# Performance work log

Measured on AMD Instinct MI355X. Metric: run time of the kernel, lower is better.

Reference implementation:

```python
import jax, jax.numpy as jnp
import numpy as np

H = 16        # attention heads
KVH = 4       # kv heads (GQA)
D = 128       # qk head_dim = qk_nope(64) + qk_rope(64)
ROPE = 64     # rotary sub-dim
VCH = 128     # v_channels
HID = 2048    # hidden size
E = 8         # routed experts
K = 2         # top-k
EPS = 1e-6
THETA = 10000.0


def rmsnorm(x, w):
    return x * jax.lax.rsqrt(jnp.mean(x * x, axis=-1, keepdims=True) + EPS) * w


def apply_rope(x, pos):
    # x: [T, h, ROPE]; rotate-half convention on the rope sub-dim
    half = ROPE // 2
    inv_freq = 1.0 / (THETA ** (jnp.arange(half, dtype=jnp.float32) / half))
    ang = pos.astype(jnp.float32)[:, None] * inv_freq          # [T, half]
    cos = jnp.cos(ang)[:, None, :]
    sin = jnp.sin(ang)[:, None, :]
    x1, x2 = x[..., :half], x[..., half:]
    return jnp.concatenate([x1 * cos - x2 * sin, x1 * sin + x2 * cos], axis=-1)


def swiglu(x, w_gate, w_up, w_down):
    return (jax.nn.silu(x @ w_gate) * (x @ w_up)) @ w_down


def setup_inputs() -> dict:
    key = jax.random.key(0)
    ks = jax.random.split(key, 16)
    T = 2048
    sc = 0.02
    n = lambda k, s: jax.random.normal(k, s, dtype=jnp.float32) * sc
    return {
        "x": jax.random.normal(ks[0], (T, HID), dtype=jnp.float32),
        "positions": jnp.arange(T, dtype=jnp.int32),
        "ln1_w": jnp.ones((HID,), jnp.float32),
        "qkv_w": n(ks[1], (HID, H * D + KVH * D + KVH * VCH)),
        "qkv_b": n(ks[2], (H * D + KVH * D + KVH * VCH,)),
        "k_ln_w": jnp.ones((D,), jnp.float32),
        "o_w": n(ks[3], (H * VCH, HID)),
        "ln2_w": jnp.ones((HID,), jnp.float32),
        "router_w": n(ks[4], (HID, E)),
        "w1": n(ks[5], (E, HID, 512)),
        "w2": n(ks[6], (E, 512, HID)),
        "w3": n(ks[7], (E, HID, 512)),
        "sw1": n(ks[8], (HID, 1024)),
        "sw2": n(ks[9], (1024, HID)),
        "sw3": n(ks[10], (HID, 1024)),
    }


def reference(x, positions, ln1_w, qkv_w, qkv_b, k_ln_w, o_w, ln2_w,
              router_w, w1, w2, w3, sw1, sw2, sw3):
    T = x.shape[0]
    # --- attention block ---
    h = rmsnorm(x, ln1_w)
    qkv = h @ qkv_w + qkv_b
    q = qkv[:, : H * D].reshape(T, H, D)
    k = qkv[:, H * D : H * D + KVH * D].reshape(T, KVH, D)
    v = qkv[:, H * D + KVH * D :].reshape(T, KVH, VCH)
    k = rmsnorm(k, k_ln_w)  # per-head k_layernorm over head_dim
    # rope applied to the trailing qk_rope_dim of q/k
    q = jnp.concatenate([q[..., : D - ROPE], apply_rope(q[..., D - ROPE :], positions)], -1)
    k = jnp.concatenate([k[..., : D - ROPE], apply_rope(k[..., D - ROPE :], positions)], -1)
    rep = H // KVH
    kf = jnp.repeat(k, rep, axis=1)   # [T, H, D]
    vf = jnp.repeat(v, rep, axis=1)   # [T, H, VCH]
    scale = D ** -0.5
    scores = jnp.einsum("qhd,khd->hqk", q, kf) * scale
    causal = jnp.tril(jnp.ones((T, T), dtype=bool))
    scores = jnp.where(causal[None], scores, jnp.float32(-1e30))
    p = jax.nn.softmax(scores, axis=-1)
    attn = jnp.einsum("hqk,khv->qhv", p, vf).reshape(T, H * VCH)
    x = x + attn @ o_w
    # --- MoE block: shared expert + top-k routed experts ---
    h2 = rmsnorm(x, ln2_w)
    probs = jax.nn.softmax(h2 @ router_w, axis=-1)            # [T, E]
    topw, topi = jax.lax.top_k(probs, K)
    topw = topw / jnp.sum(topw, axis=-1, keepdims=True)        # renormalize top-k
    combine = jnp.sum(jax.nn.one_hot(topi, E, dtype=h2.dtype) * topw[..., None], axis=1)  # [T, E]
    moe = swiglu(h2, sw1, sw3, sw2)                            # shared expert
    for e in range(E):  # small fixed expert count
        moe = moe + combine[:, e : e + 1] * swiglu(h2, w1[e], w3[e], w2[e])
    return x + moe
```

## Files before the change

kernel.cpp:

```cpp
#include <hip/hip_runtime.h>


typedef _Float16 half_t;
typedef _Float16 half8 __attribute__((ext_vector_type(8)));
typedef float    f32x4 __attribute__((ext_vector_type(4)));
typedef float    floatx4 __attribute__((ext_vector_type(4)));

#define T_TOK 2048
#define HIDN  2048
#define NH    16
#define NKVH  4
#define HD    128
#define QKV_N 3072
#define NEXP  8
#define NPAIR_MAX 4608

#define MFMA16(a,b,c) __builtin_amdgcn_mfma_f32_16x16x32_f16(a,b,c,0,0,0)

__device__ __forceinline__ void gload_lds16(const half_t* g, half_t* l) {
    __builtin_amdgcn_global_load_lds(
        (const __attribute__((address_space(1))) void*)g,
        (__attribute__((address_space(3))) void*)l, 16, 0, 0);
}

// ... 14 lines not shown
    for (int o = 32; o; o >>= 1) ss += __shfl_down(ss, o);
    __shared__ float red[4];
    if ((tid & 63) == 0) red[tid >> 6] = ss;
    __syncthreads();
    ss = red[0] + red[1] + red[2] + red[3];
    float rs = rsqrtf(ss * (1.0f / HIDN) + 1e-6f);
    floatx4 w0 = *(const floatx4*)(w + tid * 8);
    floatx4 w1 = *(const floatx4*)(w + tid * 8 + 4);
    float vv[8] = { v0[0]*w0[0], v0[1]*w0[1], v0[2]*w0[2], v0[3]*w0[3],
                    v1[0]*w1[0], v1[1]*w1[1], v1[2]*w1[2], v1[3]*w1[3] };
    half8 hv, lv;
#pragma unroll
    for (int j = 0; j < 8; ++j) {
        float o = vv[j] * rs;
        half_t h = (half_t)o;
        hv[j] = h;
        lv[j] = (half_t)((o - (float)h) * 1024.0f);
    }
    *(half8*)(hi + (size_t)row * HIDN + tid * 8) = hv;
    if (lo) *(half8*)(lo + (size_t)row * HIDN + tid * 8) = lv;
}

__global__ __launch_bounds__(256)
void transpose_split2(const float* __restrict__ src, half_t* __restrict__ dh,
                      half_t* __restrict__ dl, int sstride, int dstride)
{
    __shared__ float tile[32][36];
    const int n0 = blockIdx.x * 32, k0 = blockIdx.y * 32;
    const int tid = threadIdx.x;
    {
        int r = tid >> 3, c = (tid & 7) * 4;
        *(floatx4*)&tile[r][c] =
            *(const floatx4*)(src + (size_t)(k0 + r) * sstride + n0 + c);
    }
    __syncthreads();
    int n = tid & 31, g = tid >> 5, gg = g & 3;
    half8 hv;
    if (g < 4) {
#pragma unroll
        for (int j = 0; j < 8; ++j) hv[j] = (half_t)tile[gg * 8 + j][n];
        *(half8*)(dh + (size_t)(n0 + n) * dstride + k0 + gg * 8) = hv;
    } else {
#pragma unroll
        for (int j = 0; j < 8; ++j) {
            float v = tile[gg * 8 + j][n];
            half_t h = (half_t)v;
            hv[j] = (half_t)((v - (float)h) * 1024.0f);
        }
        *(half8*)(dl + (size_t)(n0 + n) * dstride + k0 + gg * 8) = hv;
    }
}

__global__ __launch_bounds__(256)
void transpose_f16(const float* __restrict__ src, half_t* __restrict__ dh,
                   int sstride, int dstride)
{
// ... 55 lines not shown
    const int tid = threadIdx.x;
    {
        int r = tid >> 3, c = (tid & 7) * 4;
        int k = k0 + r;
        const float* s;
        if (k < 1024) s = sw2 + (size_t)k * HIDN + n0;
        else {
            int e = (k - 1024) >> 9, kk = (k - 1024) & 511;
            s = w2 + ((size_t)e * 512 + kk) * HIDN + n0;
        }
        *(floatx4*)&tile[r][c]      = *(const floatx4*)(s + c);
        *(floatx4*)&tile[r][c + 32] = *(const floatx4*)(s + c + 32);
    }
    __syncthreads();
    int n = tid & 63, g = tid >> 6;
    half8 hv;
#pragma unroll
    for (int j = 0; j < 8; ++j) hv[j] = (half_t)tile[g * 8 + j][n];
    *(half8*)(dst + (size_t)(n0 + n) * 5120 + k0 + g * 8) = hv;
}

__global__ __launch_bounds__(256)
void owu_kernel(const float* __restrict__ ow, const float* __restrict__ ln2w,
                const float* __restrict__ rw, float* __restrict__ owu)
{
    const int k = blockIdx.x * 4 + (threadIdx.x >> 6);
    const int lane = threadIdx.x & 63;
    float acc[NEXP] = {};
    const float* row = ow + (size_t)k * HIDN;
#pragma unroll
    for (int j = 0; j < 8; ++j) {
        int c = j * 256 + lane * 4;
        floatx4 ov = *(const floatx4*)(row + c);
        floatx4 lw = *(const floatx4*)(ln2w + c);
#pragma unroll
        for (int i = 0; i < 4; ++i) {
            float s = ov[i] * lw[i];
            const float* rwc = rw + (size_t)(c + i) * NEXP;
#pragma unroll
            for (int e = 0; e < NEXP; ++e) acc[e] += s * rwc[e];
        }
    }
#pragma unroll
    for (int e = 0; e < NEXP; ++e)
        for (int o = 32; o; o >>= 1) acc[e] += __shfl_down(acc[e], o);
    if (lane == 0) {
#pragma unroll
        for (int e = 0; e < NEXP; ++e) owu[(size_t)k * NEXP + e] = acc[e];
    }
}

template<bool SPLIT, int BM>
__global__ __launch_bounds__(256, 2)
void gemm_f16(const half_t* __restrict__ Ah, const half_t* __restrict__ Al,
              const half_t* __restrict__ Bth, const half_t* __restrict__ Btl,
              const float* __restrict__ bias, const float* __restrict__ res,
              float* __restrict__ Cf, half_t* __restrict__ Ch,
              int M, int N, int K, int ldb)
{
    constexpr int NBUF = SPLIT ? 2 : 1;
    constexpr int MR = BM / 32;
    __shared__ half_t As[2][NBUF][BM * 32];
    __shared__ half_t Bs[2][NBUF][128 * 32];
    const int tid = threadIdx.x, lane = tid & 63, wid = tid >> 6;
    const int l15 = lane & 15, l4 = lane >> 4;
    const int row0 = blockIdx.y * BM, col0 = blockIdx.x * 128;
    const int wr = (wid >> 1) * (BM / 2), wc = (wid & 1) * 64;
    f32x4 accM[MR][4] = {}, accC[MR][4] = {};
    const int lrw = lane >> 2, lcl = (lane & 3) * 8;

#define STAGE(BUF, K0)                                                        \
    do {                                                                      \
        _Pragma("unroll")                                                     \
        for (int j = 0; j < BM / 64; ++j) {                                   \
            const int r = wid * (BM / 4) + j * 16;                            \
            const size_t ga = (size_t)(row0 + r + lrw) * K + (K0) + lcl;      \
            gload_lds16(Ah + ga, &As[BUF][0][r * 32]);                        \
            if constexpr (SPLIT) gload_lds16(Al + ga, &As[BUF][1][r * 32]);   \
        }                                                                     \
        _Pragma("unroll")                                                     \
        for (int j = 0; j < 2; ++j) {                                         \
            const int r = wid * 32 + j * 16;                                  \
            const size_t gb = (size_t)(col0 + r + lrw) * ldb + (K0) + lcl;    \
            gload_lds16(Bth + gb, &Bs[BUF][0][r * 32]);                       \
            if constexpr (SPLIT) gload_lds16(Btl + gb, &Bs[BUF][1][r * 32]);  \
        }                                                                     \
    } while (0)

    STAGE(0, 0);
    __syncthreads();
    int cur = 0;
    for (int k0 = 0; k0 < K; k0 += 32, cur ^= 1) {
        if (k0 + 32 < K) STAGE(cur ^ 1, k0 + 32);
        half8 ah[MR], al[MR], bh[4], bl[4];
#pragma unroll
        for (int m = 0; m < MR; ++m) {
            int off = (wr + m * 16 + l15) * 32 + l4 * 8;
            ah[m] = *(const half8*)&As[cur][0][off];
            if constexpr (SPLIT) al[m] = *(const half8*)&As[cur][1][off];
// ... 19 lines not shown
#undef STAGE

#pragma unroll
    for (int m = 0; m < MR; ++m) {
#pragma unroll
        for (int n = 0; n < 4; ++n) {
            int gr0 = row0 + wr + m * 16 + l4 * 4;
            int gc  = col0 + wc + n * 16 + l15;
            float b = bias ? bias[gc] : 0.0f;
#pragma unroll
            for (int i = 0; i < 4; ++i) {
                float v = accM[m][n][i];
                if constexpr (SPLIT) v += accC[m][n][i] * (1.0f / 1024.0f);
                v += b;
                size_t idx = (size_t)(gr0 + i) * N + gc;
                if (res) v += res[idx];
                if (Cf) Cf[idx] = v;
                if (Ch) Ch[idx] = (half_t)v;
            }
        }
    }
}

__global__ __launch_bounds__(256, 2)
void gemm_grouped_gu(const half_t* __restrict__ h2, const half_t* __restrict__ W13t,
                     const int* __restrict__ pairTok, const int* __restrict__ basep,
                     half_t* __restrict__ GUp)
{
    __shared__ half_t As[2][64 * 32];
    __shared__ half_t Bs[2][128 * 32];
    const int tid = threadIdx.x, lane = tid & 63, wid = tid >> 6;
    const int l15 = lane & 15, l4 = lane >> 4;
    const int lrw = lane >> 2, lcl = (lane & 3) * 8;
    const int row0 = blockIdx.y * 64, ct = blockIdx.x;
    int e = 0;
#pragma unroll
    for (int i = 1; i < NEXP; ++i) if (row0 >= basep[i]) e = i;
    const int brow0 = (ct < 4) ? (2048 + 512 * e + ct * 128)
                               : (6144 + 512 * e + (ct - 4) * 128);
    const int wr = (wid >> 1) * 32, wc = (wid & 1) * 64;
    const int tok = pairTok[row0 + wid * 16 + lrw];
    const half_t* Abase = h2 + (size_t)tok * HIDN + lcl;
    f32x4 acc[2][4] = {};

#define GSTAGE(BUF, K0)                                                       \
    do {                                                                      \
        gload_lds16(Abase + (K0), &As[BUF][(wid * 16) * 32]);                 \
        _Pragma("unroll")                                                     \
        for (int j = 0; j < 2; ++j) {                                         \
            const int r = wid * 32 + j * 16;                                  \
            const size_t gb = (size_t)(brow0 + r + lrw) * HIDN + (K0) + lcl;  \
            gload_lds16(W13t + gb, &Bs[BUF][r * 32]);                         \
        }                                                                     \
    } while (0)

    GSTAGE(0, 0);
    __syncthreads();
    int cur = 0;
    for (int k0 = 0; k0 < HIDN; k0 += 32, cur ^= 1) {
        if (k0 + 32 < HIDN) GSTAGE(cur ^ 1, k0 + 32);
        half8 ah[2], bh[4];
#pragma unroll
        for (int m = 0; m < 2; ++m)
            ah[m] = *(const half8*)&As[cur][(wr + m * 16 + l15) * 32 + l4 * 8];
#pragma unroll
        for (int n = 0; n < 4; ++n)
            bh[n] = *(const half8*)&Bs[cur][(wc + n * 16 + l15) * 32 + l4 * 8];
#pragma unroll
        for (int m = 0; m < 2; ++m)
#pragma unroll
            for (int n = 0; n < 4; ++n)
                acc[m][n] = MFMA16(ah[m], bh[n], acc[m][n]);
        __syncthreads();
    }
#undef GSTAGE

#pragma unroll
    for (int m = 0; m < 2; ++m)
#pragma unroll
        for (int n = 0; n < 4; ++n) {
            int gr0 = row0 + wr + m * 16 + l4 * 4;
            int gc  = ct * 128 + wc + n * 16 + l15;
#pragma unroll
            for (int i = 0; i < 4; ++i)
                GUp[(size_t)(gr0 + i) * 1024 + gc] = (half_t)acc[m][n][i];
        }
}

__global__ __launch_bounds__(256, 2)
void gemm_grouped_down(const half_t* __restrict__ Ab, const half_t* __restrict__ W2t,
                       const int* __restrict__ basep, half_t* __restrict__ Ypair)
{
    __shared__ half_t As[2][64 * 32];
    __shared__ half_t Bs[2][128 * 32];
    const int tid = threadIdx.x, lane = tid & 63, wid = tid >> 6;
    const int l15 = lane & 15, l4 = lane >> 4;
    const int lrw = lane >> 2, lcl = (lane & 3) * 8;
    const int row0 = blockIdx.y * 64, col0 = blockIdx.x * 128;
    int e = 0;
#pragma unroll
    for (int i = 1; i < NEXP; ++i) if (row0 >= basep[i]) e = i;
    const int bcol = 1024 + 512 * e;
    const int wr = (wid >> 1) * 32, wc = (wid & 1) * 64;
    f32x4 acc[2][4] = {};

#define DSTAGE(BUF, K0)                                                       \
    do {                                                                      \
        const size_t ga = (size_t)(row0 + wid * 16 + lrw) * 512 + (K0) + lcl; \
        gload_lds16(Ab + ga, &As[BUF][(wid * 16) * 32]);                      \
// ... 19 lines not shown
            bh[n] = *(const half8*)&Bs[cur][(wc + n * 16 + l15) * 32 + l4 * 8];
#pragma unroll
        for (int m = 0; m < 2; ++m)
#pragma unroll
            for (int n = 0; n < 4; ++n)
                acc[m][n] = MFMA16(ah[m], bh[n], acc[m][n]);
        __syncthreads();
    }
#undef DSTAGE

#pragma unroll
    for (int m = 0; m < 2; ++m)
#pragma unroll
        for (int n = 0; n < 4; ++n) {
            int gr0 = row0 + wr + m * 16 + l4 * 4;
            int gc  = col0 + wc + n * 16 + l15;
#pragma unroll
            for (int i = 0; i < 4; ++i)
                Ypair[(size_t)(gr0 + i) * HIDN + gc] = (half_t)acc[m][n][i];
        }
}

__global__ __launch_bounds__(256)
void qkv_prep(const float* __restrict__ qkv, const int* __restrict__ pos,
              const float* __restrict__ klnw,
              half_t* __restrict__ qh, half_t* __restrict__ ql,
              half_t* __restrict__ kh, half_t* __restrict__ kl)
{
    const int t = blockIdx.x, tid = threadIdx.x, lane = tid & 63, wid = tid >> 6;
    const float* row = qkv + (size_t)t * QKV_N;
    __shared__ float cs[32], sn[32];
    if (tid < 32) {
        double freq = exp((double)tid * -0.28782313662425572);
        double ang = (double)pos[t] * freq;
        const double twopi = 6.283185307179586476925286766559;
        ang -= twopi * floor(ang * (1.0 / twopi));
        float a = (float)ang;
        cs[tid] = cosf(a);
        sn[tid] = sinf(a);
    }
    __syncthreads();

    const float qscale = 0.08838834764831845f;
    {
        const int hh = tid >> 4, d0 = (tid & 15) * 8;
        const float* qrow = row + hh * HD;
        float outv[8];
        if (d0 < 64) {
#pragma unroll
            for (int j = 0; j < 8; ++j) outv[j] = qrow[d0 + j];
        } else if (d0 < 96) {
            int j0 = d0 - 64;
#pragma unroll
            for (int j = 0; j < 8; ++j) {
                int jj = j0 + j;
                outv[j] = qrow[64 + jj] * cs[jj] - qrow[96 + jj] * sn[jj];
            }
        } else {
            int j0 = d0 - 96;
#pragma unroll
            for (int j = 0; j < 8; ++j) {
                int jj = j0 + j;
                outv[j] = qrow[64 + jj] * sn[jj] + qrow[96 + jj] * cs[jj];
            }
        }
        half8 hv, lv;
#pragma unroll
        for (int j = 0; j < 8; ++j) {
            float o = outv[j] * qscale;
            half_t h = (half_t)o;
            hv[j] = h;
            lv[j] = (half_t)((o - (float)h) * 1024.0f);
        }
        size_t base = (size_t)t * (NH * HD) + hh * HD + d0;
        *(half8*)(qh + base) = hv;
        *(half8*)(ql + base) = lv;
    }
    {
        const float* krow = row + NH * HD + wid * HD;
        float a0 = krow[lane], a1 = krow[64 + lane];
        float ss = a0 * a0 + a1 * a1;
        for (int o = 32; o; o >>= 1) ss += __shfl_down(ss, o);
        ss = __shfl(ss, 0);
        float rs = rsqrtf(ss * (1.0f / HD) + 1e-6f);
        float n0 = a0 * rs * klnw[lane];
        float n1 = a1 * rs * klnw[64 + lane];
        float other = __shfl_xor(n1, 32);
        int j = lane & 31;
        float o1 = (lane < 32) ? (n1 * cs[j] - other * sn[j])
                               : (other * sn[j] + n1 * cs[j]);
        size_t base = (size_t)t * (NKVH * HD) + wid * HD;
        half_t h;
        h = (half_t)n0; kh[base + lane] = h;
        kl[base + lane] = (half_t)((n0 - (float)h) * 1024.0f);
        h = (half_t)o1; kh[base + 64 + lane] = h;
        kl[base + 64 + lane] = (half_t)((o1 - (float)h) * 1024.0f);
    }
}

__global__ __launch_bounds__(256, 2)
void attn_kernel(const half_t* __restrict__ qh, const half_t* __restrict__ ql,
                 const half_t* __restrict__ kh, const half_t* __restrict__ kl,
                 const half_t* __restrict__ vth, const half_t* __restrict__ vtl,
                 half_t* __restrict__ oh, half_t* __restrict__ ol,
                 float* __restrict__ Op0, float* __restrict__ Op1,
                 float* __restrict__ ml)
{
    const int bid = blockIdx.x;
    const int h = bid & 15, r = bid >> 4;
    int q, c;
    if (r < 8)       { q = r;                 c = 0; }
    else if (r < 24) { q = 8 + ((r - 8) >> 1);  c = (r - 8) & 1; }
    else if (r < 48) { q = 16 + (r - 24) / 3;   c = (r - 24) % 3; }
    else             { q = 24 + ((r - 48) >> 2); c = (r - 48) & 3; }
    const int nch = (q < 8) ? 1 : (q < 16) ? 2 : (q < 24) ? 3 : 4;
    const int nt = 2 * (q + 1);
    const int kvbeg = ((c * nt) / nch) * 32;
    const int kvend = (((c + 1) * nt) / nch) * 32;

    const int kvh = h >> 2;
    const int tid = threadIdx.x, lane = tid & 63, wid = tid >> 6;
    const int q0 = q * 64 + wid * 16;
    const int l15 = lane & 15, l4 = lane >> 4;

    __shared__ half_t Ksh[32][136], Ksl[32][136];
    __shared__ half_t Vsh[128][40], Vsl[128][40];
    __shared__ half_t Ph[4][16][40], Pl[4][16][40];

    half8 qfh[4], qfl[4];
    {
        const size_t qb = (size_t)(q0 + l15) * (NH * HD) + h * HD + l4 * 8;
#pragma unroll
        for (int cc = 0; cc < 4; ++cc) {
            qfh[cc] = *(const half8*)(qh + qb + cc * 32);
            qfl[cc] = *(const half8*)(ql + qb + cc * 32);
        }
    }

// ... 101 lines not shown
        __syncthreads();
    }
#undef LOAD_TILE

#pragma unroll
    for (int i = 0; i < 4; ++i)
#pragma unroll
        for (int o = 1; o < 16; o <<= 1) lrow[i] += __shfl_xor(lrow[i], o);

    if (nch == 1) {
#pragma unroll
        for (int c8 = 0; c8 < 8; ++c8) {
#pragma unroll
            for (int i = 0; i < 4; ++i) {
                float v = (om[c8][i] + oc[c8][i] * (1.0f / 1024.0f)) / lrow[i];
                size_t idx = (size_t)(q0 + l4 * 4 + i) * (NH * HD) + h * HD
                           + c8 * 16 + l15;
                half_t hh = (half_t)v;
                oh[idx] = hh;
                ol[idx] = (half_t)((v - (float)hh) * 1024.0f);
            }
        }
    } else {
        float* Op = (bid < 768) ? Op0 + (size_t)bid * 8192
                                : Op1 + (size_t)(bid - 768) * 8192;
#pragma unroll
        for (int c8 = 0; c8 < 8; ++c8) {
#pragma unroll
            for (int i = 0; i < 4; ++i) {
                int row64 = wid * 16 + l4 * 4 + i;
                Op[row64 * 128 + c8 * 16 + l15] =
                    om[c8][i] + oc[c8][i] * (1.0f / 1024.0f);
            }
        }
        if (l15 == 0) {
#pragma unroll
            for (int i = 0; i < 4; ++i) {
                int row64 = wid * 16 + l4 * 4 + i;
                ml[(size_t)bid * 128 + row64]      = mrow[i];
                ml[(size_t)bid * 128 + 64 + row64] = lrow[i];
            }
        }
    }
}

__global__ __launch_bounds__(256)
void attn_combine(const float* __restrict__ Op0, const float* __restrict__ Op1,
                  const float* __restrict__ ml,
                  half_t* __restrict__ oh, half_t* __restrict__ ol)
{
    const int bid = blockIdx.x;
    const int h = bid & 15, q = 8 + (bid >> 4);
    const int nch = (q < 16) ? 2 : (q < 24) ? 3 : 4;
    const int r0 = (q < 16) ? 8 + (q - 8) * 2
                 : (q < 24) ? 24 + (q - 16) * 3
                            : 48 + (q - 24) * 4;
    const int tid = threadIdx.x;
    const int row = tid >> 2, cg = (tid & 3) * 32;

    const float* Oc[4];
    float m[4], lv[4];
#pragma unroll
    for (int c = 0; c < 4; ++c) {
        int cc = (c < nch) ? c : nch - 1;
        int slot = (r0 + cc) * 16 + h;
        const float* base = (slot < 768) ? Op0 + (size_t)slot * 8192
                                         : Op1 + (size_t)(slot - 768) * 8192;
        Oc[c] = base + row * 128 + cg;
        m[c]  = ml[(size_t)slot * 128 + row];
        lv[c] = (c < nch) ? ml[(size_t)slot * 128 + 64 + row] : 0.0f;
    }
    float M = fmaxf(fmaxf(m[0], m[1]), fmaxf(m[2], m[3]));
    float w[4], wsum = 0.0f;
#pragma unroll
    for (int c = 0; c < 4; ++c) { w[c] = expf(m[c] - M); wsum += lv[c] * w[c]; }
    float inv = 1.0f / wsum;
    float wO[4];
#pragma unroll
    for (int c = 0; c < 4; ++c) wO[c] = (c < nch) ? w[c] * inv : 0.0f;

    size_t obase = (size_t)(q * 64 + row) * (NH * HD) + h * HD + cg;
#pragma unroll
    for (int jj = 0; jj < 4; ++jj) {
        floatx4 a0 = {0,0,0,0}, a1 = {0,0,0,0};
#pragma unroll
        for (int c = 0; c < 4; ++c) {
            floatx4 v0 = *(const floatx4*)(Oc[c] + jj * 8);
            floatx4 v1 = *(const floatx4*)(Oc[c] + jj * 8 + 4);
            a0 += wO[c] * v0;
            a1 += wO[c] * v1;
        }
        half8 hv, lvv;
#pragma unroll
        for (int k = 0; k < 4; ++k) {
            half_t hh = (half_t)a0[k];
            hv[k] = hh; lvv[k] = (half_t)((a0[k] - (float)hh) * 1024.0f);
            hh = (half_t)a1[k];
            hv[4 + k] = hh; lvv[4 + k] = (half_t)((a1[k] - (float)hh) * 1024.0f);
        }
        *(half8*)(oh + obase + jj * 8) = hv;
        *(half8*)(ol + obase + jj * 8) = lvv;
    }
}

__global__ __launch_bounds__(256)
void router_linear(const float* __restrict__ x, const half_t* __restrict__ ah,
                   const half_t* __restrict__ al, const float* __restrict__ x2,
                   const float* __restrict__ ln2w, const float* __restrict__ rw,
                   const float* __restrict__ owu,
                   int* __restrict__ topi, float* __restrict__ topv,
                   int* __restrict__ cnt)
{
    const int t = blockIdx.x, tid = threadIdx.x;
    const float* xr2 = x2 + (size_t)t * HIDN;
    float ss = 0.0f;
#pragma unroll
    for (int i = 0; i < 8; ++i) {
        float v = xr2[tid + i * 256];
        ss += v * v;
    }
    for (int o = 32; o; o >>= 1) ss += __shfl_down(ss, o);
    __shared__ float red[4];
    if ((tid & 63) == 0) red[tid >> 6] = ss;
    __syncthreads();
    ss = red[0] + red[1] + red[2] + red[3];
    float rs = rsqrtf(ss * (1.0f / HIDN) + 1e-6f);

    const float* xr = x + (size_t)t * HIDN;
    const half_t* ar = ah + (size_t)t * HIDN;
    const half_t* alr = al + (size_t)t * HIDN;
    float acc[NEXP] = {};
#pragma unroll
    for (int i = 0; i < 8; ++i) {
        int c = tid + i * 256;
        float xv = xr[c] * ln2w[c];
        float ap = (float)ar[c] + (float)alr[c] * (1.0f / 1024.0f);
        const float* rwc = rw + (size_t)c * NEXP;
        const float* owc = owu + (size_t)c * NEXP;
#pragma unroll
        for (int e = 0; e < NEXP; ++e) acc[e] += xv * rwc[e] + ap * owc[e];
    }
#pragma unroll
    for (int e = 0; e < NEXP; ++e)
        for (int o = 32; o; o >>= 1) acc[e] += __shfl_down(acc[e], o);
    __shared__ float red8[4][NEXP];
    if ((tid & 63) == 0)
#pragma unroll
        for (int e = 0; e < NEXP; ++e) red8[tid >> 6][e] = acc[e];
    __syncthreads();
    if (tid == 0) {
        float lg[NEXP];
#pragma unroll
        for (int e = 0; e < NEXP; ++e)
            lg[e] = (red8[0][e] + red8[1][e] + red8[2][e] + red8[3][e]) * rs;
        int i1 = 0;
        for (int e = 1; e < NEXP; ++e) if (lg[e] > lg[i1]) i1 = e;
        int i2 = (i1 == 0) ? 1 : 0;
        for (int e = 0; e < NEXP; ++e) if (e != i1 && lg[e] > lg[i2]) i2 = e;
        float mx = lg[i1];
        float p1 = expf(lg[i1] - mx), p2 = expf(lg[i2] - mx);
        float inv = 1.0f / (p1 + p2);
        topi[2 * t] = i1;     topi[2 * t + 1] = i2;
        topv[2 * t] = p1 * inv; topv[2 * t + 1] = p2 * inv;
        atomicAdd(&cnt[i1], 1);
        atomicAdd(&cnt[i2], 1);
    }
}

__global__ __launch_bounds__(256)
void moe_init(int* __restrict__ cnt, int* __restrict__ pairTok,
              float* __restrict__ pairW)
{
    int idx = blockIdx.x * 256 + threadIdx.x;
    if (idx < NPAIR_MAX) { pairTok[idx] = 0; pairW[idx] = 0.0f; }
    if (idx < NEXP) cnt[idx] = 0;
}

__global__ __launch_bounds__(64)
void moe_scan(const int* __restrict__ cnt, int* __restrict__ fill,
              int* __restrict__ basep)
{
    if (threadIdx.x == 0) {
        int acc = 0;
        for (int e = 0; e < NEXP; ++e) {
            basep[e] = acc;
            fill[e] = acc;
            acc += (cnt[e] + 63) & ~63;
        }
        basep[NEXP] = acc;
    }
}

__global__ __launch_bounds__(256)
void moe_scatter(const int* __restrict__ topi, const float* __restrict__ topv,
                 int* __restrict__ fill, int* __restrict__ pairTok,
                 float* __restrict__ pairW, int* __restrict__ pairPos)
{
    int t = blockIdx.x * 256 + threadIdx.x;
#pragma unroll
    for (int j = 0; j < 2; ++j) {
        int e = topi[2 * t + j];
        int pos = atomicAdd(&fill[e], 1);
        pairTok[pos] = t;
        pairW[pos] = topv[2 * t + j];
        pairPos[2 * t + j] = pos;
    }
}

__global__ __launch_bounds__(256)
void act_shared(const half_t* __restrict__ GUs, half_t* __restrict__ As)
{
    int idx = blockIdx.x * 256 + threadIdx.x;
    int t = idx >> 7, c = (idx & 127) * 8;
    half8 g8 = *(const half8*)(GUs + (size_t)t * 2048 + c);
    half8 u8 = *(const half8*)(GUs + (size_t)t * 2048 + 1024 + c);
    half8 o8;
#pragma unroll
    for (int j = 0; j < 8; ++j)
        o8[j] = (half_t)(silu_f((float)g8[j]) * (float)u8[j]);
    *(half8*)(As + (size_t)t * 1024 + c) = o8;
}

__global__ __launch_bounds__(256)
void act_sparse(const half_t* __restrict__ GUp, const float* __restrict__ pairW,
                half_t* __restrict__ Ab)
{
    int idx = blockIdx.x * 256 + threadIdx.x;
    int p = idx >> 6, c = (idx & 63) * 8;
    half8 g8 = *(const half8*)(GUp + (size_t)p * 1024 + c);
    half8 u8 = *(const half8*)(GUp + (size_t)p * 1024 + 512 + c);
    float w = pairW[p];
    half8 o8;
#pragma unroll
    for (int j = 0; j < 8; ++j)
        o8[j] = (half_t)(silu_f((float)g8[j]) * (float)u8[j] * w);
    *(half8*)(Ab + (size_t)p * 512 + c) = o8;
}

__global__ __launch_bounds__(256)
void moe_final(const half_t* __restrict__ Ypair, const int* __restrict__ pairPos,
               float* __restrict__ out)
{
    int t = blockIdx.x, c0 = threadIdx.x * 8;
    int p1 = pairPos[2 * t], p2 = pairPos[2 * t + 1];
    half8 y1 = *(const half8*)(Ypair + (size_t)p1 * HIDN + c0);
    half8 y2 = *(const half8*)(Ypair + (size_t)p2 * HIDN + c0);
    float* o = out + (size_t)t * HIDN + c0;
    floatx4 a = *(floatx4*)o, b = *(floatx4*)(o + 4);
#pragma unroll
    for (int j = 0; j < 4; ++j) {
        a[j] += (float)y1[j] + (float)y2[j];
        b[j] += (float)y1[4 + j] + (float)y2[4 + j];
    }
    *(floatx4*)o = a;
    *(floatx4*)(o + 4) = b;
}

extern "C" void kernel_launch(void* const* d_in, const int* in_sizes, int n_in,
                              void* d_out, int out_size, void* d_ws, size_t ws_size,
// ... 11 lines not shown
    const float* rw   = (const float*)d_in[8];
    const float* w1   = (const float*)d_in[9];
    const float* w2   = (const float*)d_in[10];
    const float* w3   = (const float*)d_in[11];
    const float* sw1  = (const float*)d_in[12];
    const float* sw2  = (const float*)d_in[13];
    const float* sw3  = (const float*)d_in[14];
    float* out = (float*)d_out;

    char* ws = (char*)d_ws;
    const size_t AB = 16842752;
    float*  x2      = (float*)(ws);
    half_t* h_hi    = (half_t*)(ws + AB);
    half_t* h_lo    = (half_t*)(ws + AB + 8388608);
    half_t* qkvwt_h = (half_t*)(ws + AB + 16777216);
    half_t* qkvwt_l = (half_t*)(ws + AB + 29360128);
    float*  qkv     = (float*)(ws + AB + 41943040);
    half_t* q_h     = (half_t*)(ws + AB + 67108864);
    half_t* q_l     = (half_t*)(ws + AB + 75497472);
    half_t* k_h     = (half_t*)(ws + AB + 83886080);
    half_t* k_l     = (half_t*)(ws + AB + 85983232);
    half_t* vt_h    = (half_t*)(ws + AB + 88080384);
    half_t* vt_l    = (half_t*)(ws + AB + 90177536);
    half_t* attn_h  = (half_t*)(ws + AB);
    half_t* attn_l  = (half_t*)(ws + AB + 8388608);
    half_t* owt     = (half_t*)(ws + AB + 16777216);
    float*  ow_u    = (float*)(ws + AB + 25165824);
    int*    cnt     = (int*)(ws + AB + 25231360);
    int*    fill    = cnt + 16;
    int*    basep   = cnt + 32;
    int*    topi    = cnt + 64;
    float*  topv    = (float*)(cnt + 4160);
    int*    pairPos = (int*)(cnt + 8256);
    int*    pairTok = (int*)(cnt + 12352);
    float*  pairW   = (float*)(cnt + 16960);
    float*  mlpart  = (float*)(ws + AB + 25231360);
    float*  Opart0  = (float*)(ws + AB + 41943040);
    float*  Opart1  = (float*)(ws);
    half_t* h2      = (half_t*)(ws + AB + 33554432);
    half_t* W13t    = (half_t*)(ws + AB + 41943040);
    half_t* GUs     = (half_t*)(ws + AB + 83886080);
    half_t* As_sh   = (half_t*)(ws + AB);
    half_t* GUp     = (half_t*)(ws + AB + 4194304);
    half_t* Ab      = (half_t*)(ws + AB + 16777216);
    half_t* W2t     = (half_t*)(ws + AB + 41943040);
    half_t* Ypair   = (half_t*)(ws + AB + 92274688);

    dim3 b256(256);

    rmsnorm_split_k<<<T_TOK, b256, 0, stream>>>(x, ln1w, h_hi, h_lo);
    transpose_split2<<<dim3(QKV_N / 32, HIDN / 32), b256, 0, stream>>>(
        qkvw, qkvwt_h, qkvwt_l, QKV_N, HIDN);
    gemm_f16<true, 64><<<dim3(QKV_N / 128, T_TOK / 64), b256, 0, stream>>>(
        h_hi, h_lo, qkvwt_h, qkvwt_l, qkvb, nullptr, qkv, nullptr,
        T_TOK, QKV_N, HIDN, HIDN);
    qkv_prep<<<T_TOK, b256, 0, stream>>>(qkv, pos, klnw, q_h, q_l, k_h, k_l);
    transpose_split2<<<dim3(512 / 32, T_TOK / 32), b256, 0, stream>>>(
        qkv + 2560, vt_h, vt_l, QKV_N, T_TOK);
    transpose_f16<<<dim3(HIDN / 64, HIDN / 32), b256, 0, stream>>>(
        ow, owt, HIDN, HIDN);
    owu_kernel<<<512, b256, 0, stream>>>(ow, ln2w, rw, ow_u);
    attn_kernel<<<1280, b256, 0, stream>>>(
        q_h, q_l, k_h, k_l, vt_h, vt_l, attn_h, attn_l,
        Opart0, Opart1, mlpart);
    attn_combine<<<384, b256, 0, stream>>>(Opart0, Opart1, mlpart,
                                           attn_h, attn_l);
    gemm_f16<false, 64><<<dim3(HIDN / 128, T_TOK / 64), b256, 0, stream>>>(
        attn_h, nullptr, owt, nullptr, nullptr, x, x2, nullptr,
        T_TOK, HIDN, HIDN, HIDN);
    moe_init<<<18, b256, 0, stream>>>(cnt, pairTok, pairW);
    router_linear<<<T_TOK, b256, 0, stream>>>(
        x, attn_h, attn_l, x2, ln2w, rw, ow_u, topi, topv, cnt);
    moe_scan<<<1, 64, 0, stream>>>(cnt, fill, basep);
    moe_scatter<<<NEXP, b256, 0, stream>>>(topi, topv, fill,
                                           pairTok, pairW, pairPos);
    rmsnorm_split_k<<<T_TOK, b256, 0, stream>>>(x2, ln2w, h2, nullptr);
    w13_transpose<<<dim3(10240 / 64, HIDN / 32), b256, 0, stream>>>(
        sw1, w1, sw3, w3, W13t);
    gemm_f16<false, 64><<<dim3(2048 / 128, T_TOK / 64), b256, 0, stream>>>(
        h2, nullptr, W13t, nullptr, nullptr, nullptr, nullptr, GUs,
        T_TOK, 2048, HIDN, HIDN);
    gemm_grouped_gu<<<dim3(8, NPAIR_MAX / 64), b256, 0, stream>>>(
        h2, W13t, pairTok, basep, GUp);
    act_shared<<<(T_TOK * 128) / 256, b256, 0, stream>>>(GUs, As_sh);
    act_sparse<<<(NPAIR_MAX * 64) / 256, b256, 0, stream>>>(GUp, pairW, Ab);
    w2_transpose<<<dim3(HIDN / 64, 5120 / 32), b256, 0, stream>>>(sw2, w2, W2t);
    gemm_f16<false, 64><<<dim3(HIDN / 128, T_TOK / 64), b256, 0, stream>>>(
        As_sh, nullptr, W2t, nullptr, nullptr, x2, out, nullptr,
        T_TOK, HIDN, 1024, 5120);
    gemm_grouped_down<<<dim3(16, NPAIR_MAX / 64), b256, 0, stream>>>(
        Ab, W2t, basep, Ypair);
    moe_final<<<T_TOK, b256, 0, stream>>>(Ypair, pairPos, out);
}
```

Before: 622.2 us.

## Split-K QKV GEMM, fuse SwiGLU activation into gate/up GEMMs, rebalance attention chunks

The QKV projection GEMM is split along K into two halves written to separate buffers, which are summed inside qkv_prep and the V transpose. This doubles the grid so more CUs are busy. SiLU-times-up activation is fused into the gate/up GEMM epilogues through an LDS exchange tile, removing the act_shared/act_sparse kernels and their intermediate round trips. The ln2 rmsnorm is fused into router_linear, moe_init is folded into owu_kernel, and attention work is redistributed into finer KV chunks (up to 6 per query block) with a generic combine. The costs are extra partial-buffer traffic and a looped, non-unrolled combine.

```diff
diff --git a/kernel.cpp b/kernel.cpp
--- a/kernel.cpp
+++ b/kernel.cpp
@@ -60,16 +60,19 @@
 }
 
 __global__ __launch_bounds__(256)
-void transpose_split2(const float* __restrict__ src, half_t* __restrict__ dh,
-                      half_t* __restrict__ dl, int sstride, int dstride)
+void transpose_split2(const float* __restrict__ src, const float* __restrict__ src2,
+                      half_t* __restrict__ dh, half_t* __restrict__ dl,
+                      int sstride, int dstride)
 {
     __shared__ float tile[32][36];
     const int n0 = blockIdx.x * 32, k0 = blockIdx.y * 32;
     const int tid = threadIdx.x;
     {
         int r = tid >> 3, c = (tid & 7) * 4;
-        *(floatx4*)&tile[r][c] =
-            *(const floatx4*)(src + (size_t)(k0 + r) * sstride + n0 + c);
+        size_t off = (size_t)(k0 + r) * sstride + n0 + c;
+        floatx4 v = *(const floatx4*)(src + off);
+        if (src2) v += *(const floatx4*)(src2 + off);
+        *(floatx4*)&tile[r][c] = v;
     }
     __syncthreads();
     int n = tid & 31, g = tid >> 5, gg = g & 3;
@@ -171,8 +174,15 @@
 
 __global__ __launch_bounds__(256)
 void owu_kernel(const float* __restrict__ ow, const float* __restrict__ ln2w,
-                const float* __restrict__ rw, float* __restrict__ owu)
-{
+                const float* __restrict__ rw, float* __restrict__ owu,
+                int* __restrict__ cnt, int* __restrict__ pairTok,
+                float* __restrict__ pairW)
+{
+    if (blockIdx.x < 18) {
+        int idx = blockIdx.x * 256 + threadIdx.x;
+        if (idx < NPAIR_MAX) { pairTok[idx] = 0; pairW[idx] = 0.0f; }
+        if (idx < NEXP) cnt[idx] = 0;
+    }
     const int k = blockIdx.x * 4 + (threadIdx.x >> 6);
     const int lane = threadIdx.x & 63;
     float acc[NEXP] = {};
@@ -205,7 +215,8 @@
               const half_t* __restrict__ Bth, const half_t* __restrict__ Btl,
               const float* __restrict__ bias, const float* __restrict__ res,
               float* __restrict__ Cf, half_t* __restrict__ Ch,
-              int M, int N, int K, int ldb)
+              int M, int N, int K, int lda, int ldb,
+              float* __restrict__ Cf2)
 {
     constexpr int NBUF = SPLIT ? 2 : 1;
     constexpr int MR = BM / 32;
@@ -213,7 +224,16 @@
     __shared__ half_t Bs[2][NBUF][128 * 32];
     const int tid = threadIdx.x, lane = tid & 63, wid = tid >> 6;
     const int l15 = lane & 15, l4 = lane >> 4;
-    const int row0 = blockIdx.y * BM, col0 = blockIdx.x * 128;
+    int by = blockIdx.y;
+    if (Cf2) {
+        int kh = by >> 5; by &= 31;
+        if (kh) {
+            Ah += 1024; if (SPLIT) Al += 1024;
+            Bth += 1024; if (SPLIT) Btl += 1024;
+            Cf = Cf2; bias = nullptr;
+        }
+    }
+    const int row0 = by * BM, col0 = blockIdx.x * 128;
     const int wr = (wid >> 1) * (BM / 2), wc = (wid & 1) * 64;
     f32x4 accM[MR][4] = {}, accC[MR][4] = {};
     const int lrw = lane >> 2, lcl = (lane & 3) * 8;
@@ -223,7 +243,7 @@
         _Pragma("unroll")                                                     \
         for (int j = 0; j < BM / 64; ++j) {                                   \
             const int r = wid * (BM / 4) + j * 16;                            \
-            const size_t ga = (size_t)(row0 + r + lrw) * K + (K0) + lcl;      \
+            const size_t ga = (size_t)(row0 + r + lrw) * lda + (K0) + lcl;    \
             gload_lds16(Ah + ga, &As[BUF][0][r * 32]);                        \
             if constexpr (SPLIT) gload_lds16(Al + ga, &As[BUF][1][r * 32]);   \
         }                                                                     \
@@ -289,25 +309,38 @@
     }
 }
 
+template<bool GROUPED>
 __global__ __launch_bounds__(256, 2)
-void gemm_grouped_gu(const half_t* __restrict__ h2, const half_t* __restrict__ W13t,
-                     const int* __restrict__ pairTok, const int* __restrict__ basep,
-                     half_t* __restrict__ GUp)
+void gemm_gu_act(const half_t* __restrict__ h2, const half_t* __restrict__ W13t,
+                 const int* __restrict__ pairTok, const int* __restrict__ basep,
+                 const float* __restrict__ pairW, half_t* __restrict__ outp)
 {
     __shared__ half_t As[2][64 * 32];
     __shared__ half_t Bs[2][128 * 32];
+    __shared__ half_t ex[64][136];
     const int tid = threadIdx.x, lane = tid & 63, wid = tid >> 6;
     const int l15 = lane & 15, l4 = lane >> 4;
     const int lrw = lane >> 2, lcl = (lane & 3) * 8;
-    const int row0 = blockIdx.y * 64, ct = blockIdx.x;
-    int e = 0;
-#pragma unroll
-    for (int i = 1; i < NEXP; ++i) if (row0 >= basep[i]) e = i;
-    const int brow0 = (ct < 4) ? (2048 + 512 * e + ct * 128)
-                               : (6144 + 512 * e + (ct - 4) * 128);
+    const int ct = blockIdx.x, row0 = blockIdx.y * 64;
+    int gbase, ubase;
+    if constexpr (GROUPED) {
+        int e = 0;
+#pragma unroll
+        for (int i = 1; i < NEXP; ++i) if (row0 >= basep[i]) e = i;
+        gbase = 2048 + 512 * e + ct * 64;
+        ubase = 6144 + 512 * e + ct * 64;
+    } else {
+        gbase = ct * 64;
+        ubase = 1024 + ct * 64;
+    }
     const int wr = (wid >> 1) * 32, wc = (wid & 1) * 64;
-    const int tok = pairTok[row0 + wid * 16 + lrw];
-    const half_t* Abase = h2 + (size_t)tok * HIDN + lcl;
+    const half_t* Abase;
+    if constexpr (GROUPED) {
+        const int tok = pairTok[row0 + wid * 16 + lrw];
+        Abase = h2 + (size_t)tok * HIDN + lcl;
+    } else {
+        Abase = h2 + (size_t)(row0 + wid * 16 + lrw) * HIDN + lcl;
+    }
     f32x4 acc[2][4] = {};
 
 #define GSTAGE(BUF, K0)                                                       \
@@ -316,7 +349,8 @@
         _Pragma("unroll")                                                     \
         for (int j = 0; j < 2; ++j) {                                         \
             const int r = wid * 32 + j * 16;                                  \
-            const size_t gb = (size_t)(brow0 + r + lrw) * HIDN + (K0) + lcl;  \
+            const int grow = (r < 64) ? gbase + r : ubase + (r - 64);         \
+            const size_t gb = (size_t)(grow + lrw) * HIDN + (K0) + lcl;       \
             gload_lds16(W13t + gb, &Bs[BUF][r * 32]);                         \
         }                                                                     \
     } while (0)
@@ -345,13 +379,26 @@
 #pragma unroll
     for (int m = 0; m < 2; ++m)
 #pragma unroll
-        for (int n = 0; n < 4; ++n) {
-            int gr0 = row0 + wr + m * 16 + l4 * 4;
-            int gc  = ct * 128 + wc + n * 16 + l15;
+        for (int n = 0; n < 4; ++n)
 #pragma unroll
             for (int i = 0; i < 4; ++i)
-                GUp[(size_t)(gr0 + i) * 1024 + gc] = (half_t)acc[m][n][i];
-        }
+                ex[wr + m * 16 + l4 * 4 + i][wc + n * 16 + l15] =
+                    (half_t)acc[m][n][i];
+    __syncthreads();
+    constexpr int OSTR = GROUPED ? 512 : 1024;
+#pragma unroll
+    for (int w2 = 0; w2 < 2; ++w2) {
+        int unit = tid * 2 + w2;
+        int row = unit >> 3, cgx = (unit & 7) * 8;
+        half8 g8 = *(const half8*)&ex[row][cgx];
+        half8 u8 = *(const half8*)&ex[row][64 + cgx];
+        float wgt = GROUPED ? pairW[row0 + row] : 1.0f;
+        half8 o8;
+#pragma unroll
+        for (int j = 0; j < 8; ++j)
+            o8[j] = (half_t)(silu_f((float)g8[j]) * (float)u8[j] * wgt);
+        *(half8*)(outp + (size_t)(row0 + row) * OSTR + ct * 64 + cgx) = o8;
+    }
 }
 
 __global__ __launch_bounds__(256, 2)
@@ -417,13 +464,14 @@
 }
 
 __global__ __launch_bounds__(256)
-void qkv_prep(const float* __restrict__ qkv, const int* __restrict__ pos,
-              const float* __restrict__ klnw,
+void qkv_prep(const float* __restrict__ qkv, const float* __restrict__ qkv2,
+              const int* __restrict__ pos, const float* __restrict__ klnw,
               half_t* __restrict__ qh, half_t* __restrict__ ql,
               half_t* __restrict__ kh, half_t* __restrict__ kl)
 {
     const int t = blockIdx.x, tid = threadIdx.x, lane = tid & 63, wid = tid >> 6;
-    const float* row = qkv + (size_t)t * QKV_N;
+    const float* row  = qkv  + (size_t)t * QKV_N;
+    const float* row2 = qkv2 + (size_t)t * QKV_N;
     __shared__ float cs[32], sn[32];
     if (tid < 32) {
         double freq = exp((double)tid * -0.28782313662425572);
@@ -436,27 +484,28 @@
     }
     __syncthreads();
 
+#define QV(i) (row[i] + row2[i])
     const float qscale = 0.08838834764831845f;
     {
         const int hh = tid >> 4, d0 = (tid & 15) * 8;
-        const float* qrow = row + hh * HD;
+        const int qb = hh * HD;
         float outv[8];
         if (d0 < 64) {
 #pragma unroll
-            for (int j = 0; j < 8; ++j) outv[j] = qrow[d0 + j];
+            for (int j = 0; j < 8; ++j) outv[j] = QV(qb + d0 + j);
         } else if (d0 < 96) {
             int j0 = d0 - 64;
 #pragma unroll
             for (int j = 0; j < 8; ++j) {
                 int jj = j0 + j;
-                outv[j] = qrow[64 + jj] * cs[jj] - qrow[96 + jj] * sn[jj];
+                outv[j] = QV(qb + 64 + jj) * cs[jj] - QV(qb + 96 + jj) * sn[jj];
             }
         } else {
             int j0 = d0 - 96;
 #pragma unroll
             for (int j = 0; j < 8; ++j) {
                 int jj = j0 + j;
-                outv[j] = qrow[64 + jj] * sn[jj] + qrow[96 + jj] * cs[jj];
+                outv[j] = QV(qb + 64 + jj) * sn[jj] + QV(qb + 96 + jj) * cs[jj];
             }
         }
         half8 hv, lv;
@@ -472,8 +521,8 @@
         *(half8*)(ql + base) = lv;
     }
     {
-        const float* krow = row + NH * HD + wid * HD;
-        float a0 = krow[lane], a1 = krow[64 + lane];
+        const int kb = NH * HD + wid * HD;
+        float a0 = QV(kb + lane), a1 = QV(kb + 64 + lane);
         float ss = a0 * a0 + a1 * a1;
         for (int o = 32; o; o >>= 1) ss += __shfl_down(ss, o);
         ss = __shfl(ss, 0);
@@ -491,6 +540,7 @@
         h = (half_t)o1; kh[base + 64 + lane] = h;
         kl[base + 64 + lane] = (half_t)((o1 - (float)h) * 1024.0f);
     }
+#undef QV
 }
 
 __global__ __launch_bounds__(256, 2)
@@ -499,16 +549,16 @@
                  const half_t* __restrict__ vth, const half_t* __restrict__ vtl,
                  half_t* __restrict__ oh, half_t* __restrict__ ol,
                  float* __restrict__ Op0, float* __restrict__ Op1,
-                 float* __restrict__ ml)
+                 float* __restrict__ Op2, float* __restrict__ ml)
 {
     const int bid = blockIdx.x;
-    const int h = bid & 15, r = bid >> 4;
-    int q, c;
-    if (r < 8)       { q = r;                 c = 0; }
-    else if (r < 24) { q = 8 + ((r - 8) >> 1);  c = (r - 8) & 1; }
-    else if (r < 48) { q = 16 + (r - 24) / 3;   c = (r - 24) % 3; }
-    else             { q = 24 + ((r - 48) >> 2); c = (r - 48) & 3; }
-    const int nch = (q < 8) ? 1 : (q < 16) ? 2 : (q < 24) ? 3 : 4;
+    const int h = bid & 15;
+    int rrem = bid >> 4, q = 31, nch = 6, c = 0;
+    for (; q >= 0; --q) {
+        nch = (q + 6) / 6;
+        if (rrem < nch) { c = rrem; break; }
+        rrem -= nch;
+    }
     const int nt = 2 * (q + 1);
     const int kvbeg = ((c * nt) / nch) * 32;
     const int kvend = (((c + 1) * nt) / nch) * 32;
@@ -656,8 +706,9 @@
             }
         }
     } else {
-        float* Op = (bid < 768) ? Op0 + (size_t)bid * 8192
-                                : Op1 + (size_t)(bid - 768) * 8192;
+        float* Op = (bid < 768)  ? Op0 + (size_t)bid * 8192
+                  : (bid < 1280) ? Op1 + (size_t)(bid - 768) * 8192
+                                 : Op2 + (size_t)(bid - 1280) * 8192;
 #pragma unroll
         for (int c8 = 0; c8 < 8; ++c8) {
 #pragma unroll
@@ -678,51 +729,51 @@
     }
 }
 
+__device__ __forceinline__ const float* slot_ptr(int s, const float* Op0,
+                                                 const float* Op1,
+                                                 const float* Op2)
+{
+    return (s < 768)  ? Op0 + (size_t)s * 8192
+         : (s < 1280) ? Op1 + (size_t)(s - 768) * 8192
+                      : Op2 + (size_t)(s - 1280) * 8192;
+}
+
 __global__ __launch_bounds__(256)
 void attn_combine(const float* __restrict__ Op0, const float* __restrict__ Op1,
-                  const float* __restrict__ ml,
+                  const float* __restrict__ Op2, const float* __restrict__ ml,
                   half_t* __restrict__ oh, half_t* __restrict__ ol)
 {
     const int bid = blockIdx.x;
-    const int h = bid & 15, q = 8 + (bid >> 4);
-    const int nch = (q < 16) ? 2 : (q < 24) ? 3 : 4;
-    const int r0 = (q < 16) ? 8 + (q - 8) * 2
-                 : (q < 24) ? 24 + (q - 16) * 3
-                            : 48 + (q - 24) * 4;
+    const int h = bid & 15, q = 6 + (bid >> 4);
+    const int nch = (q + 6) / 6;
+    int r0 = 0;
+    for (int j = 31; j > q; --j) r0 += (j + 6) / 6;
     const int tid = threadIdx.x;
     const int row = tid >> 2, cg = (tid & 3) * 32;
 
-    const float* Oc[4];
-    float m[4], lv[4];
-#pragma unroll
-    for (int c = 0; c < 4; ++c) {
-        int cc = (c < nch) ? c : nch - 1;
-        int slot = (r0 + cc) * 16 + h;
-        const float* base = (slot < 768) ? Op0 + (size_t)slot * 8192
-                                         : Op1 + (size_t)(slot - 768) * 8192;
-        Oc[c] = base + row * 128 + cg;
-        m[c]  = ml[(size_t)slot * 128 + row];
-        lv[c] = (c < nch) ? ml[(size_t)slot * 128 + 64 + row] : 0.0f;
-    }
-    float M = fmaxf(fmaxf(m[0], m[1]), fmaxf(m[2], m[3]));
-    float w[4], wsum = 0.0f;
-#pragma unroll
-    for (int c = 0; c < 4; ++c) { w[c] = expf(m[c] - M); wsum += lv[c] * w[c]; }
+    float M = -1e30f;
+    for (int c = 0; c < nch; ++c) {
+        int s = (r0 + c) * 16 + h;
+        M = fmaxf(M, ml[(size_t)s * 128 + row]);
+    }
+    float wsum = 0.0f;
+    for (int c = 0; c < nch; ++c) {
+        int s = (r0 + c) * 16 + h;
+        wsum += ml[(size_t)s * 128 + 64 + row] *
+                expf(ml[(size_t)s * 128 + row] - M);
+    }
     float inv = 1.0f / wsum;
-    float wO[4];
-#pragma unroll
-    for (int c = 0; c < 4; ++c) wO[c] = (c < nch) ? w[c] * inv : 0.0f;
 
     size_t obase = (size_t)(q * 64 + row) * (NH * HD) + h * HD + cg;
 #pragma unroll
     for (int jj = 0; jj < 4; ++jj) {
         floatx4 a0 = {0,0,0,0}, a1 = {0,0,0,0};
-#pragma unroll
-        for (int c = 0; c < 4; ++c) {
-            floatx4 v0 = *(const floatx4*)(Oc[c] + jj * 8);
-            floatx4 v1 = *(const floatx4*)(Oc[c] + jj * 8 + 4);
-            a0 += wO[c] * v0;
-            a1 += wO[c] * v1;
+        for (int c = 0; c < nch; ++c) {
+            int s = (r0 + c) * 16 + h;
+            float w = expf(ml[(size_t)s * 128 + row] - M) * inv;
+            const float* base = slot_ptr(s, Op0, Op1, Op2) + row * 128 + cg;
+            a0 += w * (*(const floatx4*)(base + jj * 8));
+            a1 += w * (*(const floatx4*)(base + jj * 8 + 4));
         }
         half8 hv, lvv;
 #pragma unroll
@@ -743,16 +794,14 @@
                    const float* __restrict__ ln2w, const float* __restrict__ rw,
                    const float* __restrict__ owu,
                    int* __restrict__ topi, float* __restrict__ topv,
-                   int* __restrict__ cnt)
+                   int* __restrict__ cnt, half_t* __restrict__ h2)
 {
     const int t = blockIdx.x, tid = threadIdx.x;
-    const float* xr2 = x2 + (size_t)t * HIDN;
-    float ss = 0.0f;
-#pragma unroll
-    for (int i = 0; i < 8; ++i) {
-        float v = xr2[tid + i * 256];
-        ss += v * v;
-    }
+    const float* xr2 = x2 + (size_t)t * HIDN + tid * 8;
+    floatx4 x2a = *(const floatx4*)(xr2);
+    floatx4 x2b = *(const floatx4*)(xr2 + 4);
+    float ss = x2a[0]*x2a[0] + x2a[1]*x2a[1] + x2a[2]*x2a[2] + x2a[3]*x2a[3]
+             + x2b[0]*x2b[0] + x2b[1]*x2b[1] + x2b[2]*x2b[2] + x2b[3]*x2b[3];
     for (int o = 32; o; o >>= 1) ss += __shfl_down(ss, o);
     __shared__ float red[4];
     if ((tid & 63) == 0) red[tid >> 6] = ss;
@@ -760,15 +809,20 @@
     ss = red[0] + red[1] + red[2] + red[3];
     float rs = rsqrtf(ss * (1.0f / HIDN) + 1e-6f);
 
-    const float* xr = x + (size_t)t * HIDN;
-    const half_t* ar = ah + (size_t)t * HIDN;
-    const half_t* alr = al + (size_t)t * HIDN;
+    const float* xr = x + (size_t)t * HIDN + tid * 8;
+    floatx4 xa = *(const floatx4*)(xr);
+    floatx4 xb = *(const floatx4*)(xr + 4);
+    floatx4 lwa = *(const floatx4*)(ln2w + tid * 8);
+    floatx4 lwb = *(const floatx4*)(ln2w + tid * 8 + 4);
+    half8 av  = *(const half8*)(ah + (size_t)t * HIDN + tid * 8);
+    half8 alv = *(const half8*)(al + (size_t)t * HIDN + tid * 8);
+
     float acc[NEXP] = {};
 #pragma unroll
-    for (int i = 0; i < 8; ++i) {
-        int c = tid + i * 256;
-        float xv = xr[c] * ln2w[c];
-        float ap = (float)ar[c] + (float)alr[c] * (1.0f / 1024.0f);
+    for (int j = 0; j < 8; ++j) {
+        int c = tid * 8 + j;
+        float xv = (j < 4 ? xa[j] : xb[j - 4]) * (j < 4 ? lwa[j] : lwb[j - 4]);
+        float ap = (float)av[j] + (float)alv[j] * (1.0f / 1024.0f);
         const float* rwc = rw + (size_t)c * NEXP;
         const float* owc = owu + (size_t)c * NEXP;
 #pragma unroll
@@ -781,6 +835,15 @@
     if ((tid & 63) == 0)
 #pragma unroll
         for (int e = 0; e < NEXP; ++e) red8[tid >> 6][e] = acc[e];
+
+    half8 h2v;
+#pragma unroll
+    for (int j = 0; j < 8; ++j) {
+        float xv = (j < 4 ? x2a[j] : x2b[j - 4]) * (j < 4 ? lwa[j] : lwb[j - 4]);
+        h2v[j] = (half_t)(xv * rs);
+    }
+    *(half8*)(h2 + (size_t)t * HIDN + tid * 8) = h2v;
+
     __syncthreads();
     if (tid == 0) {
         float lg[NEXP];
@@ -794,20 +857,11 @@
         float mx = lg[i1];
         float p1 = expf(lg[i1] - mx), p2 = expf(lg[i2] - mx);
         float inv = 1.0f / (p1 + p2);
-        topi[2 * t] = i1;     topi[2 * t + 1] = i2;
+        topi[2 * t] = i1;       topi[2 * t + 1] = i2;
         topv[2 * t] = p1 * inv; topv[2 * t + 1] = p2 * inv;
         atomicAdd(&cnt[i1], 1);
         atomicAdd(&cnt[i2], 1);
     }
-}
-
-__global__ __launch_bounds__(256)
-void moe_init(int* __restrict__ cnt, int* __restrict__ pairTok,
-              float* __restrict__ pairW)
-{
-    int idx = blockIdx.x * 256 + threadIdx.x;
-    if (idx < NPAIR_MAX) { pairTok[idx] = 0; pairW[idx] = 0.0f; }
-    if (idx < NEXP) cnt[idx] = 0;
 }
 
 __global__ __launch_bounds__(64)
@@ -839,36 +893,6 @@
         pairW[pos] = topv[2 * t + j];
         pairPos[2 * t + j] = pos;
     }
-}
-
-__global__ __launch_bounds__(256)
-void act_shared(const half_t* __restrict__ GUs, half_t* __restrict__ As)
-{
-    int idx = blockIdx.x * 256 + threadIdx.x;
-    int t = idx >> 7, c = (idx & 127) * 8;
-    half8 g8 = *(const half8*)(GUs + (size_t)t * 2048 + c);
-    half8 u8 = *(const half8*)(GUs + (size_t)t * 2048 + 1024 + c);
-    half8 o8;
-#pragma unroll
-    for (int j = 0; j < 8; ++j)
-        o8[j] = (half_t)(silu_f((float)g8[j]) * (float)u8[j]);
-    *(half8*)(As + (size_t)t * 1024 + c) = o8;
-}
-
-__global__ __launch_bounds__(256)
-void act_sparse(const half_t* __restrict__ GUp, const float* __restrict__ pairW,
-                half_t* __restrict__ Ab)
-{
-    int idx = blockIdx.x * 256 + threadIdx.x;
-    int p = idx >> 6, c = (idx & 63) * 8;
-    half8 g8 = *(const half8*)(GUp + (size_t)p * 1024 + c);
-    half8 u8 = *(const half8*)(GUp + (size_t)p * 1024 + 512 + c);
-    float w = pairW[p];
-    half8 o8;
-#pragma unroll
-    for (int j = 0; j < 8; ++j)
-        o8[j] = (half_t)(silu_f((float)g8[j]) * (float)u8[j] * w);
-    *(half8*)(Ab + (size_t)p * 512 + c) = o8;
 }
 
 __global__ __launch_bounds__(256)
@@ -926,72 +950,71 @@
     half_t* k_l     = (half_t*)(ws + AB + 85983232);
     half_t* vt_h    = (half_t*)(ws + AB + 88080384);
     half_t* vt_l    = (half_t*)(ws + AB + 90177536);
+    float*  qkv2    = (float*)(ws + AB + 92274688);
     half_t* attn_h  = (half_t*)(ws + AB);
     half_t* attn_l  = (half_t*)(ws + AB + 8388608);
     half_t* owt     = (half_t*)(ws + AB + 16777216);
     float*  ow_u    = (float*)(ws + AB + 25165824);
-    int*    cnt     = (int*)(ws + AB + 25231360);
-    int*    fill    = cnt + 16;
-    int*    basep   = cnt + 32;
-    int*    topi    = cnt + 64;
-    float*  topv    = (float*)(cnt + 4160);
-    int*    pairPos = (int*)(cnt + 8256);
-    int*    pairTok = (int*)(cnt + 12352);
-    float*  pairW   = (float*)(cnt + 16960);
     float*  mlpart  = (float*)(ws + AB + 25231360);
     float*  Opart0  = (float*)(ws + AB + 41943040);
     float*  Opart1  = (float*)(ws);
+    float*  Opart2  = (float*)(ws + AB + 29360128);
     half_t* h2      = (half_t*)(ws + AB + 33554432);
     half_t* W13t    = (half_t*)(ws + AB + 41943040);
-    half_t* GUs     = (half_t*)(ws + AB + 83886080);
     half_t* As_sh   = (half_t*)(ws + AB);
-    half_t* GUp     = (half_t*)(ws + AB + 4194304);
     half_t* Ab      = (half_t*)(ws + AB + 16777216);
     half_t* W2t     = (half_t*)(ws + AB + 41943040);
     half_t* Ypair   = (half_t*)(ws + AB + 92274688);
 
+    char* meta = ws + (size_t)(AB + 117440512);
+    int*    cnt     = (int*)  (meta + 0);
+    int*    fill    = (int*)  (meta + 64);
+    int*    basep   = (int*)  (meta + 128);
+    int*    topi    = (int*)  (meta + 256);
+    float*  topv    = (float*)(meta + 16640);
+    int*    pairPos = (int*)  (meta + 33024);
+    int*    pairTok = (int*)  (meta + 49408);
+    float*  pairW   = (float*)(meta + 67840);
+
     dim3 b256(256);
 
     rmsnorm_split_k<<<T_TOK, b256, 0, stream>>>(x, ln1w, h_hi, h_lo);
     transpose_split2<<<dim3(QKV_N / 32, HIDN / 32), b256, 0, stream>>>(
-        qkvw, qkvwt_h, qkvwt_l, QKV_N, HIDN);
-    gemm_f16<true, 64><<<dim3(QKV_N / 128, T_TOK / 64), b256, 0, stream>>>(
+        qkvw, nullptr, qkvwt_h, qkvwt_l, QKV_N, HIDN);
+    gemm_f16<true, 64><<<dim3(QKV_N / 128, 64), b256, 0, stream>>>(
         h_hi, h_lo, qkvwt_h, qkvwt_l, qkvb, nullptr, qkv, nullptr,
-        T_TOK, QKV_N, HIDN, HIDN);
-    qkv_prep<<<T_TOK, b256, 0, stream>>>(qkv, pos, klnw, q_h, q_l, k_h, k_l);
+        T_TOK, QKV_N, 1024, HIDN, HIDN, qkv2);
+    qkv_prep<<<T_TOK, b256, 0, stream>>>(qkv, qkv2, pos, klnw,
+                                         q_h, q_l, k_h, k_l);
     transpose_split2<<<dim3(512 / 32, T_TOK / 32), b256, 0, stream>>>(
-        qkv + 2560, vt_h, vt_l, QKV_N, T_TOK);
+        qkv + 2560, qkv2 + 2560, vt_h, vt_l, QKV_N, T_TOK);
     transpose_f16<<<dim3(HIDN / 64, HIDN / 32), b256, 0, stream>>>(
         ow, owt, HIDN, HIDN);
-    owu_kernel<<<512, b256, 0, stream>>>(ow, ln2w, rw, ow_u);
-    attn_kernel<<<1280, b256, 0, stream>>>(
+    owu_kernel<<<512, b256, 0, stream>>>(ow, ln2w, rw, ow_u,
+                                         cnt, pairTok, pairW);
+    attn_kernel<<<1632, b256, 0, stream>>>(
         q_h, q_l, k_h, k_l, vt_h, vt_l, attn_h, attn_l,
-        Opart0, Opart1, mlpart);
-    attn_combine<<<384, b256, 0, stream>>>(Opart0, Opart1, mlpart,
+        Opart0, Opart1, Opart2, mlpart);
+    attn_combine<<<416, b256, 0, stream>>>(Opart0, Opart1, Opart2, mlpart,
                                            attn_h, attn_l);
     gemm_f16<false, 64><<<dim3(HIDN / 128, T_TOK / 64), b256, 0, stream>>>(
         attn_h, nullptr, owt, nullptr, nullptr, x, x2, nullptr,
-        T_TOK, HIDN, HIDN, HIDN);
-    moe_init<<<18, b256, 0, stream>>>(cnt, pairTok, pairW);
+        T_TOK, HIDN, HIDN, HIDN, HIDN, nullptr);
     router_linear<<<T_TOK, b256, 0, stream>>>(
-        x, attn_h, attn_l, x2, ln2w, rw, ow_u, topi, topv, cnt);
+        x, attn_h, attn_l, x2, ln2w, rw, ow_u, topi, topv, cnt, h2);
     moe_scan<<<1, 64, 0, stream>>>(cnt, fill, basep);
     moe_scatter<<<NEXP, b256, 0, stream>>>(topi, topv, fill,
                                            pairTok, pairW, pairPos);
-    rmsnorm_split_k<<<T_TOK, b256, 0, stream>>>(x2, ln2w, h2, nullptr);
     w13_transpose<<<dim3(10240 / 64, HIDN / 32), b256, 0, stream>>>(
         sw1, w1, sw3, w3, W13t);
-    gemm_f16<false, 64><<<dim3(2048 / 128, T_TOK / 64), b256, 0, stream>>>(
-        h2, nullptr, W13t, nullptr, nullptr, nullptr, nullptr, GUs,
-        T_TOK, 2048, HIDN, HIDN);
-    gemm_grouped_gu<<<dim3(8, NPAIR_MAX / 64), b256, 0, stream>>>(
-        h2, W13t, pairTok, basep, GUp);
-    act_shared<<<(T_TOK * 128) / 256, b256, 0, stream>>>(GUs, As_sh);
-    act_sparse<<<(NPAIR_MAX * 64) / 256, b256, 0, stream>>>(GUp, pairW, Ab);
+    gemm_gu_act<false><<<dim3(16, T_TOK / 64), b256, 0, stream>>>(
+        h2, W13t, nullptr, nullptr, nullptr, As_sh);
+    gemm_gu_act<true><<<dim3(8, NPAIR_MAX / 64), b256, 0, stream>>>(
+        h2, W13t, pairTok, basep, pairW, Ab);
     w2_transpose<<<dim3(HIDN / 64, 5120 / 32), b256, 0, stream>>>(sw2, w2, W2t);
     gemm_f16<false, 64><<<dim3(HIDN / 128, T_TOK / 64), b256, 0, stream>>>(
         As_sh, nullptr, W2t, nullptr, nullptr, x2, out, nullptr,
-        T_TOK, HIDN, 1024, 5120);
+        T_TOK, HIDN, 1024, 1024, 5120, nullptr);
     gemm_grouped_down<<<dim3(16, NPAIR_MAX / 64), b256, 0, stream>>>(
         Ab, W2t, basep, Ypair);
     moe_final<<<T_TOK, b256, 0, stream>>>(Ypair, pairPos, out);
```

New measurement: 650.6 us. 4.6% more time.
